# Kernel optimization log

Hardware: AMD Instinct MI355X
Metric: run time of the kernel (lower is better)

The kernel has to match this reference:

```python
import jax, jax.numpy as jnp
import numpy as np

STRIDE = 8  # window over x[:, max(0, i-stride) : i+1]


def setup_inputs() -> dict:
    key = jax.random.key(0)
    k0, k1, k2, k3, k4 = jax.random.split(key, 5)
    B, T, H = 16, 8192, 256
    x = jax.random.normal(k0, (B, T, H), dtype=jnp.float32)
    s = 1.0 / np.sqrt(H)  # torch nn.Linear default init range
    W_lin = jax.random.uniform(k1, (H, H), jnp.float32, -s, s)
    b_lin = jax.random.uniform(k2, (H,), jnp.float32, -s, s)
    W_mem = jax.random.uniform(k3, (H, H), jnp.float32, -s, s)
    b_mem = jax.random.uniform(k4, (H,), jnp.float32, -s, s)
    return {"x": x, "W_lin": W_lin, "b_lin": b_lin, "W_mem": W_mem, "b_mem": b_mem}


def reference(x, W_lin, b_lin, W_mem, b_mem):
    # x: [B, T, H]; input_dim == hidden_dim so input_lin is None in the original.
    B, T, H = x.shape
    # h = Linear(x)  (torch Linear: x @ W.T + b)
    h = jnp.einsum('bth,oh->bto', x, W_lin) + b_lin
    # Causal sliding-window mean over window [max(0, t-STRIDE), t] via cumsum.
    cs = jnp.cumsum(x, axis=1)                       # [B, T, H]
    idx = jnp.arange(T)
    start = jnp.maximum(0, idx - STRIDE)             # [T]
    prev = jnp.where((start > 0)[None, :, None],
                     cs[:, jnp.maximum(start - 1, 0)], 0.0)
    counts = (idx - start + 1).astype(x.dtype)       # min(t+1, STRIDE+1)
    means = (cs - prev) / counts[None, :, None]      # [B, T, H]
    # memory branch: Linear over window means, batched as one matmul
    mem = jnp.einsum('bth,oh->bto', means, W_mem) + b_mem
    return h + mem
```

## Files before the change

kernel.cpp:

```cpp
#include <hip/hip_runtime.h>
#include <hip/hip_bf16.h>

#define B_ 16
#define T_ 8192
#define H_ 256
#define M_ (B_ * T_)
#define STRIDE_ 8

typedef __bf16 bf16x8 __attribute__((ext_vector_type(8)));
typedef float f32x4 __attribute__((ext_vector_type(4)));

__device__ __forceinline__ unsigned short f2bf(float f) {
  unsigned u = __builtin_bit_cast(unsigned, f);
  u += 0x7fffu + ((u >> 16) & 1u);
  return (unsigned short)(u >> 16);
}

__device__ __forceinline__ void load_lds16(const void* g, void* l) {
  __builtin_amdgcn_global_load_lds(
      (const __attribute__((address_space(1))) void*)g,
      (__attribute__((address_space(3))) void*)l, 16, 0, 0);
}

__global__ __launch_bounds__(256) void wcat_kernel(
    const float* __restrict__ Wl, const float* __restrict__ bl,
    const float* __restrict__ Wm, const float* __restrict__ bm,
    unsigned short* __restrict__ Wpk, float* __restrict__ bias) {
  const int e = blockIdx.x * 256 + threadIdx.x;
  const int it = e >> 14;
  const int r = (e >> 6) & 255;
  const int col = e & 63;
  const int cp = col >> 3;
  const int ei = col & 7;
  const int c = cp ^ (r & 7);
  const int k = it * 32 + (c & 3) * 8 + ei + ((c < 4) ? 0 : 256);
  const float w = (k < 256) ? Wl[r * 256 + k] : Wm[r * 256 + (k - 256)];
  Wpk[e] = f2bf(w);
  if (e < 256) bias[e] = bl[e] + bm[e];
}

__global__ __launch_bounds__(256, 3) void fused_kernel(
    const float* __restrict__ x,
    const unsigned short* __restrict__ Wpk,
    const float* __restrict__ bias,
    float* __restrict__ out) {
  __shared__ __align__(16) unsigned short As[64 * 64];
  __shared__ __align__(16) unsigned short Bs[256 * 64];
  const int tid = threadIdx.x;
  const int m0 = blockIdx.x << 6;
  const int tb0 = m0 & (T_ - 1);
  const int w = tid >> 6;
  const int l = tid & 63;
  const int wc = w << 6;
  const int lm = l & 15;
  const int kqc = l >> 4;

  const int p = tid & 15, g = tid >> 4;
  const float2* __restrict__ x2 = (const float2*)x;
  unsigned* __restrict__ As32 = (unsigned*)As;

  f32x4 acc[4][4];
#pragma unroll
  for (int i = 0; i < 4; ++i)
#pragma unroll
    for (int j = 0; j < 4; ++j) acc[i][j] = (f32x4){0.f, 0.f, 0.f, 0.f};

  for (int it = 0; it < 8; ++it) {
    __syncthreads();

    const unsigned short* bsrc = Wpk + (it << 14);
#pragma unroll
    for (int rnd = 0; rnd < 8; ++rnd) {
      const int f = tid + (rnd << 8);
      load_lds16(bsrc + f * 8, &Bs[f * 8]);
    }

    float2 v[12];
#pragma unroll
    for (int i = 0; i < 12; ++i) {
      const int rl = (g << 2) - 8 + i;
      float2 val = {0.f, 0.f};
      if (tb0 + rl >= 0)
        val = x2[(size_t)(m0 + rl) * 128 + (it << 4) + p];
      v[i] = val;
    }
    float sx = 0.f, sy = 0.f;
#pragma unroll
    for (int i = 0; i < 8; ++i) { sx += v[i].x; sy += v[i].y; }
#pragma unroll
    for (int rr = 0; rr < 4; ++rr) {
      sx += v[rr + 8].x; sy += v[rr + 8].y;
      const int r = (g << 2) + rr;
      const int t = tb0 + r;
      const float inv =
          (t >= STRIDE_) ? (1.f / 9.f) : __builtin_amdgcn_rcpf((float)(t + 1));
      const unsigned xp =
          (unsigned)f2bf(v[rr + 8].x) | ((unsigned)f2bf(v[rr + 8].y) << 16);
      const unsigned mp =
          (unsigned)f2bf(sx * inv) | ((unsigned)f2bf(sy * inv) << 16);
      const int sw = r & 7;
      As32[r * 32 + (((p >> 2) ^ sw) << 2) + (p & 3)] = xp;
      As32[r * 32 + (((4 + (p >> 2)) ^ sw) << 2) + (p & 3)] = mp;
      sx -= v[rr].x; sy -= v[rr].y;
    }
    __syncthreads();

#pragma unroll
    for (int kk = 0; kk < 2; ++kk) {
      const int cc = (kk << 2) + kqc;
      bf16x8 a[4], bb[4];
#pragma unroll
      for (int i = 0; i < 4; ++i) {
        const int R = (i << 4) + lm;
        a[i] = *(const bf16x8*)&As[R * 64 + ((cc ^ (R & 7)) << 3)];
      }
#pragma unroll
      for (int j = 0; j < 4; ++j) {
        const int R = wc + (j << 4) + lm;
        bb[j] = *(const bf16x8*)&Bs[R * 64 + ((cc ^ (R & 7)) << 3)];
      }
#pragma unroll
      for (int i = 0; i < 4; ++i)
#pragma unroll
        for (int j = 0; j < 4; ++j)
          acc[i][j] = __builtin_amdgcn_mfma_f32_16x16x32_bf16(a[i], bb[j],
                                                              acc[i][j], 0, 0, 0);
    }
  }

  const int r0 = (l >> 4) << 2;
#pragma unroll
  for (int j = 0; j < 4; ++j) {
    const int o = wc + (j << 4) + lm;
    const float bs = bias[o];
#pragma unroll
    for (int i = 0; i < 4; ++i) {
      const size_t mr = (size_t)(m0 + (i << 4) + r0);
#pragma unroll
      for (int r = 0; r < 4; ++r) out[(mr + r) * 256 + o] = acc[i][j][r] + bs;
    }
  }
}

extern "C" void kernel_launch(void* const* d_in, const int* in_sizes, int n_in,
                              void* d_out, int out_size, void* d_ws, size_t ws_size,
                              hipStream_t stream) {
  const float* x  = (const float*)d_in[0];
  const float* Wl = (const float*)d_in[1];
  const float* bl = (const float*)d_in[2];
  const float* Wm = (const float*)d_in[3];
  const float* bm = (const float*)d_in[4];
  float* out = (float*)d_out;

  char* ws = (char*)d_ws;
  unsigned short* Wpk = (unsigned short*)ws;
  float* bias = (float*)(ws + (size_t)8 * 256 * 64 * 2);

  wcat_kernel<<<512, 256, 0, stream>>>(Wl, bl, Wm, bm, Wpk, bias);
  fused_kernel<<<2048, 256, 0, stream>>>(x, Wpk, bias, out);
}
```

Baseline: 270.4 us.

## Load weights directly from global, double-buffer A tile and prefetch next x slice

The weight tile is no longer staged through LDS. Each wave now reads its B fragments straight from a repacked global layout (k-slab major, contiguous 32-element rows), which relies on L2/L1 caching. The A tile is double-buffered so only one barrier per k-step is needed. The next iteration's x slice is prefetched into registers while the MFMAs run. This cuts LDS use and synchronisation, but adds global-load latency on the MFMA critical path and more register pressure.

```diff
diff --git a/kernel.cpp b/kernel.cpp
--- a/kernel.cpp
+++ b/kernel.cpp
@@ -16,25 +16,16 @@
   return (unsigned short)(u >> 16);
 }
 
-__device__ __forceinline__ void load_lds16(const void* g, void* l) {
-  __builtin_amdgcn_global_load_lds(
-      (const __attribute__((address_space(1))) void*)g,
-      (__attribute__((address_space(3))) void*)l, 16, 0, 0);
-}
-
 __global__ __launch_bounds__(256) void wcat_kernel(
     const float* __restrict__ Wl, const float* __restrict__ bl,
     const float* __restrict__ Wm, const float* __restrict__ bm,
     unsigned short* __restrict__ Wpk, float* __restrict__ bias) {
   const int e = blockIdx.x * 256 + threadIdx.x;
-  const int it = e >> 14;
-  const int r = (e >> 6) & 255;
-  const int col = e & 63;
-  const int cp = col >> 3;
-  const int ei = col & 7;
-  const int c = cp ^ (r & 7);
-  const int k = it * 32 + (c & 3) * 8 + ei + ((c < 4) ? 0 : 256);
-  const float w = (k < 256) ? Wl[r * 256 + k] : Wm[r * 256 + (k - 256)];
+  const int ks = e >> 13;
+  const int n = (e >> 5) & 255;
+  const int kk = e & 31;
+  const int k = ks * 32 + kk;
+  const float w = (k < 256) ? Wl[n * 256 + k] : Wm[n * 256 + (k - 256)];
   Wpk[e] = f2bf(w);
   if (e < 256) bias[e] = bl[e] + bm[e];
 }
@@ -44,8 +35,7 @@
     const unsigned short* __restrict__ Wpk,
     const float* __restrict__ bias,
     float* __restrict__ out) {
-  __shared__ __align__(16) unsigned short As[64 * 64];
-  __shared__ __align__(16) unsigned short Bs[256 * 64];
+  __shared__ __align__(16) unsigned short As[2][64 * 64];
   const int tid = threadIdx.x;
   const int m0 = blockIdx.x << 6;
   const int tb0 = m0 & (T_ - 1);
@@ -53,11 +43,11 @@
   const int l = tid & 63;
   const int wc = w << 6;
   const int lm = l & 15;
-  const int kqc = l >> 4;
+  const int kc4 = l >> 4;
+  const int kq = kc4 << 3;
 
   const int p = tid & 15, g = tid >> 4;
   const float2* __restrict__ x2 = (const float2*)x;
-  unsigned* __restrict__ As32 = (unsigned*)As;
 
   f32x4 acc[4][4];
 #pragma unroll
@@ -65,25 +55,19 @@
 #pragma unroll
     for (int j = 0; j < 4; ++j) acc[i][j] = (f32x4){0.f, 0.f, 0.f, 0.f};
 
+  float2 v[12];
+#pragma unroll
+  for (int i = 0; i < 12; ++i) {
+    const int rl = (g << 2) - 8 + i;
+    float2 val = {0.f, 0.f};
+    if (tb0 + rl >= 0) val = x2[(size_t)(m0 + rl) * 128 + p];
+    v[i] = val;
+  }
+
   for (int it = 0; it < 8; ++it) {
-    __syncthreads();
+    const int cur = it & 1;
+    unsigned* __restrict__ As32 = (unsigned*)As[cur];
 
-    const unsigned short* bsrc = Wpk + (it << 14);
-#pragma unroll
-    for (int rnd = 0; rnd < 8; ++rnd) {
-      const int f = tid + (rnd << 8);
-      load_lds16(bsrc + f * 8, &Bs[f * 8]);
-    }
-
-    float2 v[12];
-#pragma unroll
-    for (int i = 0; i < 12; ++i) {
-      const int rl = (g << 2) - 8 + i;
-      float2 val = {0.f, 0.f};
-      if (tb0 + rl >= 0)
-        val = x2[(size_t)(m0 + rl) * 128 + (it << 4) + p];
-      v[i] = val;
-    }
     float sx = 0.f, sy = 0.f;
 #pragma unroll
     for (int i = 0; i < 8; ++i) { sx += v[i].x; sy += v[i].y; }
@@ -105,27 +89,41 @@
     }
     __syncthreads();
 
+    const size_t bb0 = ((size_t)it << 13) + (wc + lm) * 32 + kq;
+    const size_t bb1 = bb0 + ((size_t)8 << 13);
+    bf16x8 b0[4], b1[4], a0[4], a1[4];
 #pragma unroll
-    for (int kk = 0; kk < 2; ++kk) {
-      const int cc = (kk << 2) + kqc;
-      bf16x8 a[4], bb[4];
+    for (int j = 0; j < 4; ++j) b0[j] = *(const bf16x8*)&Wpk[bb0 + (j << 9)];
 #pragma unroll
-      for (int i = 0; i < 4; ++i) {
-        const int R = (i << 4) + lm;
-        a[i] = *(const bf16x8*)&As[R * 64 + ((cc ^ (R & 7)) << 3)];
+    for (int j = 0; j < 4; ++j) b1[j] = *(const bf16x8*)&Wpk[bb1 + (j << 9)];
+#pragma unroll
+    for (int i = 0; i < 4; ++i) {
+      const int R = (i << 4) + lm;
+      a0[i] = *(const bf16x8*)&As[cur][R * 64 + ((kc4 ^ (R & 7)) << 3)];
+      a1[i] = *(const bf16x8*)&As[cur][R * 64 + (((4 + kc4) ^ (R & 7)) << 3)];
+    }
+    if (it < 7) {
+#pragma unroll
+      for (int i = 0; i < 12; ++i) {
+        const int rl = (g << 2) - 8 + i;
+        float2 val = {0.f, 0.f};
+        if (tb0 + rl >= 0)
+          val = x2[(size_t)(m0 + rl) * 128 + ((it + 1) << 4) + p];
+        v[i] = val;
       }
+    }
 #pragma unroll
-      for (int j = 0; j < 4; ++j) {
-        const int R = wc + (j << 4) + lm;
-        bb[j] = *(const bf16x8*)&Bs[R * 64 + ((cc ^ (R & 7)) << 3)];
-      }
+    for (int i = 0; i < 4; ++i)
 #pragma unroll
-      for (int i = 0; i < 4; ++i)
+      for (int j = 0; j < 4; ++j)
+        acc[i][j] =
+            __builtin_amdgcn_mfma_f32_16x16x32_bf16(a0[i], b0[j], acc[i][j], 0, 0, 0);
 #pragma unroll
-        for (int j = 0; j < 4; ++j)
-          acc[i][j] = __builtin_amdgcn_mfma_f32_16x16x32_bf16(a[i], bb[j],
-                                                              acc[i][j], 0, 0, 0);
-    }
+    for (int i = 0; i < 4; ++i)
+#pragma unroll
+      for (int j = 0; j < 4; ++j)
+        acc[i][j] =
+            __builtin_amdgcn_mfma_f32_16x16x32_bf16(a1[i], b1[j], acc[i][j], 0, 0, 0);
   }
 
   const int r0 = (l >> 4) << 2;
@@ -154,7 +152,7 @@
 
   char* ws = (char*)d_ws;
   unsigned short* Wpk = (unsigned short*)ws;
-  float* bias = (float*)(ws + (size_t)8 * 256 * 64 * 2);
+  float* bias = (float*)(ws + (size_t)16 * 256 * 32 * 2);
 
   wcat_kernel<<<512, 256, 0, stream>>>(Wl, bl, Wm, bm, Wpk, bias);
   fused_kernel<<<2048, 256, 0, stream>>>(x, Wpk, bias, out);
```

After: 317.2 us. +17.3%, slower.
